# Kernel optimization log

Measured on AMD Instinct MI355X. Metric: run time of the kernel, lower is better.

Reference implementation:

```python
import jax, jax.numpy as jnp
import numpy as np

BINS = 10


def _neg_pearson(p, t):
    # global standardization (torch.std default is unbiased, ddof=1)
    p = (p - p.mean()) / p.std(ddof=1)
    t = (t - t.mean()) / t.std(ddof=1)
    N = p.shape[1]
    sx = p.sum(1); sy = t.sum(1)
    sxy = (p * t).sum(1)
    sx2 = (p * p).sum(1); sy2 = (t * t).sum(1)
    pear = (N * sxy - sx * sy) / jnp.sqrt((N * sx2 - sx**2) * (N * sy2 - sy**2))
    return (1.0 - pear).mean()


def _hann(N):
    # torch.hann_window is periodic: 0.5*(1 - cos(2*pi*n/N))
    return 0.5 * (1.0 - jnp.cos(2.0 * jnp.pi * jnp.arange(N, dtype=jnp.float32) / N))


def _phase_correlation(x, t):
    # torch.stft with n_fft=seq_len, center=False, hann window -> single frame = rfft(x*hann)
    N = x.shape[1]
    w = _hann(N)
    xf = jnp.fft.rfft(x * w, axis=1)   # [B, N//2+1]
    tf = jnp.fft.rfft(t * w, axis=1)
    corr = xf * jnp.conj(tf)
    corr = corr / jnp.abs(corr)        # phase-only correlation
    cm = jnp.fft.irfft(corr, n=N, axis=1)  # [B, N]
    idx = jnp.argmax(cm, axis=1)
    return 1.0 - jnp.mean(jnp.cos(2.0 * jnp.pi * idx / N))


def _power_spectrum(x, t):
    xp = jnp.abs(jnp.fft.rfft(x, axis=1)) ** 2
    tp = jnp.abs(jnp.fft.rfft(t, axis=1)) ** 2
    return jnp.mean(jnp.abs(xp - tp)) / jnp.mean(tp)


def _mutual_information(x, y, bins=BINS):
    B, S = x.shape
    xmin = x.min(1); xmax = x.max(1)
    ymin = y.min(1); ymax = y.max(1)
    bwx = (xmax - xmin) / bins
    bwy = (ymax - ymin) / bins
    ix = jnp.clip(((x - xmin[:, None]) / bwx[:, None]).astype(jnp.int32), 0, bins - 1)
    iy = jnp.clip(((y - ymin[:, None]) / bwy[:, None]).astype(jnp.int32), 0, bins - 1)
    flat = ix * bins + iy  # [B, S]
    # vectorized 2D histogram via scatter-add (replaces the python double loop)
    hist = jax.vmap(lambda f: jnp.zeros(bins * bins, jnp.float32).at[f].add(1.0))(flat)
    hist = hist.reshape(B, bins, bins)
    hx = hist.sum(2); hy = hist.sum(1)
    denom = B * S  # NOTE: original normalizes by batch*seq (faithful reproduction)
    px = hx / denom; py = hy / denom; pxy = hist / denom
    eps = 1e-8
    mi = (pxy * jnp.log((pxy + eps) / (px[:, :, None] * py[:, None, :] + eps))).sum((1, 2))
    hxe = -(px * jnp.log(px + eps)).sum(1)
    hye = -(py * jnp.log(py + eps)).sum(1)
    nmi = mi / ((hxe + hye) / 2.0)
    return 1.0 - nmi.mean()


def setup_inputs() -> dict:
    key = jax.random.key(0)
    k1, k2 = jax.random.split(key)
    return {
        "predictions": jax.random.normal(k1, (2, 512, 16384), dtype=jnp.float32),
        "targets": jax.random.normal(k2, (512, 16384), dtype=jnp.float32),
        "i": 0,
        "epoch": 700,
    }


def reference(predictions, targets, i, epoch):
    p = predictions[i]  # [B, S]
    loss = _neg_pearson(p, targets)
    if epoch >= 400:
        loss = loss + _phase_correlation(p, targets)
        loss = loss + _power_spectrum(p, targets)
    if epoch >= 700:
        loss = loss + _mutual_information(p, targets)
    return loss
```

## Files before the change

kernel.cpp:

```cpp
#include <hip/hip_runtime.h>
#include <math.h>

#define BB 512
#define SS 16384
#define TPIF 6.28318530717958647692f

#define PD(i) ((i) + ((i) >> 4) + ((i) >> 8))
#define NPD 17472
#define BBASE 8200

__device__ __forceinline__ int sp(int k) {
    int s = ((k & 7) << 11) + (((k >> 3) & 7) << 8) + (((k >> 6) & 7) << 5)
          + (((k >> 9) & 7) << 2) + ((k >> 12) & 3);
    return PD(s);
}


template <int SGN, int LOG2Q, bool DOMI = false>
__device__ __forceinline__ void stage_dif8(float2* sz, int t,
                                           float x0 = 0.f, float sbx = 0.f,
                                           float y0 = 0.f, float sby = 0.f,
                                           int* hsub = nullptr) {
    constexpr int Q = 1 << LOG2Q;
    constexpr int DQ = Q + (Q >> 4) + (Q >> 8);
    const float sg = (float)SGN;
    const float r2 = 0.70710678118654752f;
    float arev = sg * (float)(t & (Q - 1)) * (1.0f / (8.0f * (float)Q));
    float cb = __builtin_amdgcn_cosf(arev);
    float sb = __builtin_amdgcn_sinf(arev);
    #pragma unroll 1
    for (int c = 0; c < 2; ++c) {
        const int j = t + (c << 10);
        const int g = j >> LOG2Q;
        const int p = j & (Q - 1);
        const int i0 = PD((g << (LOG2Q + 3)) + p);
        int idx[8];
        #pragma unroll
        for (int k = 0; k < 8; ++k)
            idx[k] = (LOG2Q >= 4) ? (i0 + k * DQ) : (i0 + 4 * k + (k >> 2));
        float2 z[8];
        #pragma unroll
        for (int k = 0; k < 8; ++k) z[k] = sz[idx[k]];
        if constexpr (DOMI) {
            #pragma unroll
            for (int k = 0; k < 8; ++k) {
                int ix = (int)((z[k].x - x0) * sbx); ix = min(max(ix, 0), 9);
                int iy = (int)((z[k].y - y0) * sby); iy = min(max(iy, 0), 9);
                atomicAdd(&hsub[ix * 10 + iy], 1);
            }
        }
        float2 a0, a1, a2, a3, b0, b1, b2, b3;
        a0 = make_float2(z[0].x + z[4].x, z[0].y + z[4].y);
        b0 = make_float2(z[0].x - z[4].x, z[0].y - z[4].y);
        a1 = make_float2(z[1].x + z[5].x, z[1].y + z[5].y);
        b1 = make_float2(z[1].x - z[5].x, z[1].y - z[5].y);
        a2 = make_float2(z[2].x + z[6].x, z[2].y + z[6].y);
        b2 = make_float2(z[2].x - z[6].x, z[2].y - z[6].y);
        a3 = make_float2(z[3].x + z[7].x, z[3].y + z[7].y);
        b3 = make_float2(z[3].x - z[7].x, z[3].y - z[7].y);
        { float x = b1.x, y = b1.y; b1 = make_float2(r2 * (x - sg * y), r2 * (y + sg * x)); }
        { float x = b2.x, y = b2.y; b2 = make_float2(-sg * y, sg * x); }
        { float x = b3.x, y = b3.y; b3 = make_float2(-r2 * (x + sg * y), r2 * (sg * x - y)); }
        float2 o[8];
        {
            float t0r = a0.x + a2.x, t0i = a0.y + a2.y;
            float t1r = a0.x - a2.x, t1i = a0.y - a2.y;
            float t2r = a1.x + a3.x, t2i = a1.y + a3.y;
            float t3r = a1.x - a3.x, t3i = a1.y - a3.y;
            o[0] = make_float2(t0r + t2r, t0i + t2i);
            o[4] = make_float2(t0r - t2r, t0i - t2i);
            o[2] = make_float2(t1r - sg * t3i, t1i + sg * t3r);
            o[6] = make_float2(t1r + sg * t3i, t1i - sg * t3r);
        }
        {
            float t0r = b0.x + b2.x, t0i = b0.y + b2.y;
            float t1r = b0.x - b2.x, t1i = b0.y - b2.y;
            float t2r = b1.x + b3.x, t2i = b1.y + b3.y;
            float t3r = b1.x - b3.x, t3i = b1.y - b3.y;
            o[1] = make_float2(t0r + t2r, t0i + t2i);
            o[5] = make_float2(t0r - t2r, t0i - t2i);
            o[3] = make_float2(t1r - sg * t3i, t1i + sg * t3r);
            o[7] = make_float2(t1r + sg * t3i, t1i - sg * t3r);
        }
        sz[idx[0]] = o[0];
        float wr = cb, wi = sb;
        #pragma unroll
        for (int r = 1; r < 8; ++r) {
            sz[idx[r]] = make_float2(o[r].x * wr - o[r].y * wi,
                                     o[r].x * wi + o[r].y * wr);
            float nr = wr * cb - wi * sb, ni = wr * sb + wi * cb;
            wr = nr; wi = ni;
        }
        if constexpr (LOG2Q == 11) {
            const float cs = 0.92387953251128674f;
            const float sn = 0.38268343236508977f * (float)SGN;
            float nb = cb * cs - sb * sn, nsb = cb * sn + sb * cs;
            cb = nb; sb = nsb;
        }
    }
    __syncthreads();
}

template <int SGN>
__device__ __forceinline__ void stage_nt4(float2* sz, int t) {
    const float sg = (float)SGN;
    #pragma unroll 1
    for (int c = 0; c < 4; ++c) {
        const int j = t + (c << 10);
        const int i0 = 4 * j + (j >> 2) + (j >> 6);
        float2 z0 = sz[i0], z1 = sz[i0 + 1], z2 = sz[i0 + 2], z3 = sz[i0 + 3];
        float t0r = z0.x + z2.x, t0i = z0.y + z2.y;
        float t1r = z0.x - z2.x, t1i = z0.y - z2.y;
        float t2r = z1.x + z3.x, t2i = z1.y + z3.y;
        float t3r = z1.x - z3.x, t3i = z1.y - z3.y;
        sz[i0]     = make_float2(t0r + t2r, t0i + t2i);
        sz[i0 + 2] = make_float2(t0r - t2r, t0i - t2i);
        sz[i0 + 1] = make_float2(t1r - sg * t3i, t1i + sg * t3r);
        sz[i0 + 3] = make_float2(t1r + sg * t3i, t1i - sg * t3r);
    }
    __syncthreads();
}

template <int SGN, int LOG2Q>
__device__ __forceinline__ void stage8k_dif8(float2* bz, int t) {
    constexpr int Q = 1 << LOG2Q;
    constexpr int DQ = Q + (Q >> 4) + (Q >> 8);
    constexpr int CORR = (LOG2Q == 7) ? 1 : 0;
    const float sg = (float)SGN;
    const float r2 = 0.70710678118654752f;
    const int g = t >> LOG2Q;
    const int p = t & (Q - 1);
    const int i0 = PD((g << (LOG2Q + 3)) + p);
    int idx[8];
    #pragma unroll
    for (int k = 0; k < 8; ++k) idx[k] = i0 + k * DQ + CORR * (k >> 1);
    float2 z[8];
    #pragma unroll
    for (int k = 0; k < 8; ++k) z[k] = bz[idx[k]];
    float2 a0, a1, a2, a3, b0, b1, b2, b3;
    a0 = make_float2(z[0].x + z[4].x, z[0].y + z[4].y);
    b0 = make_float2(z[0].x - z[4].x, z[0].y - z[4].y);
    a1 = make_float2(z[1].x + z[5].x, z[1].y + z[5].y);
    b1 = make_float2(z[1].x - z[5].x, z[1].y - z[5].y);
    a2 = make_float2(z[2].x + z[6].x, z[2].y + z[6].y);
    b2 = make_float2(z[2].x - z[6].x, z[2].y - z[6].y);
    a3 = make_float2(z[3].x + z[7].x, z[3].y + z[7].y);
    b3 = make_float2(z[3].x - z[7].x, z[3].y - z[7].y);
    { float x = b1.x, y = b1.y; b1 = make_float2(r2 * (x - sg * y), r2 * (y + sg * x)); }
    { float x = b2.x, y = b2.y; b2 = make_float2(-sg * y, sg * x); }
    { float x = b3.x, y = b3.y; b3 = make_float2(-r2 * (x + sg * y), r2 * (sg * x - y)); }
    float2 o[8];
    {
        float t0r = a0.x + a2.x, t0i = a0.y + a2.y;
        float t1r = a0.x - a2.x, t1i = a0.y - a2.y;
        float t2r = a1.x + a3.x, t2i = a1.y + a3.y;
        float t3r = a1.x - a3.x, t3i = a1.y - a3.y;
        o[0] = make_float2(t0r + t2r, t0i + t2i);
        o[4] = make_float2(t0r - t2r, t0i - t2i);
        o[2] = make_float2(t1r - sg * t3i, t1i + sg * t3r);
        o[6] = make_float2(t1r + sg * t3i, t1i - sg * t3r);
    }
    {
        float t0r = b0.x + b2.x, t0i = b0.y + b2.y;
        float t1r = b0.x - b2.x, t1i = b0.y - b2.y;
        float t2r = b1.x + b3.x, t2i = b1.y + b3.y;
        float t3r = b1.x - b3.x, t3i = b1.y - b3.y;
        o[1] = make_float2(t0r + t2r, t0i + t2i);
        o[5] = make_float2(t0r - t2r, t0i - t2i);
        o[3] = make_float2(t1r - sg * t3i, t1i + sg * t3r);
        o[7] = make_float2(t1r + sg * t3i, t1i - sg * t3r);
    }
    const float arev = sg * (float)p * (1.0f / (8.0f * (float)Q));
    const float cb = __builtin_amdgcn_cosf(arev);
    const float sb = __builtin_amdgcn_sinf(arev);
    bz[idx[0]] = o[0];
    float wr = cb, wi = sb;
    #pragma unroll
    for (int r = 1; r < 8; ++r) {
        bz[idx[r]] = make_float2(o[r].x * wr - o[r].y * wi,
                                 o[r].x * wi + o[r].y * wr);
        float nr = wr * cb - wi * sb, ni = wr * sb + wi * cb;
        wr = nr; wi = ni;
    }
    __syncthreads();
}

__device__ __forceinline__ void inv_first(float2* sz, float2* bz, int t) {
    const float r2 = 0.70710678118654752f;
    float2 z[8];
    {
        float a0w = (float)t * (1.0f / 16384.0f);
        float wr = __builtin_amdgcn_cosf(a0w);
        float wi = __builtin_amdgcn_sinf(a0w);
        const float cs = 0.92387953251128674f;
        const float sn = 0.38268343236508977f;
        #pragma unroll
        for (int c = 0; c < 8; ++c) {
            int m = t + (c << 10);
            float2 cm = sz[m];
            float2 cn = sz[8192 - m];
            float Ax = cm.x + cn.x, Ay = cm.y - cn.y;
            float Dx = cm.x - cn.x, Dy = cm.y + cn.y;
            float WDx = Dx * wr - Dy * wi;
            float WDy = Dx * wi + Dy * wr;
            z[c] = make_float2(Ax - WDy, Ay + WDx);
            float nr = wr * cs - wi * sn, ni = wr * sn + wi * cs;
            wr = nr; wi = ni;
        }
    }
    const float sg = 1.0f;
    const int i0 = PD(t);
    float2 a0, a1, a2, a3, b0, b1, b2, b3;
    a0 = make_float2(z[0].x + z[4].x, z[0].y + z[4].y);
    b0 = make_float2(z[0].x - z[4].x, z[0].y - z[4].y);
    a1 = make_float2(z[1].x + z[5].x, z[1].y + z[5].y);
    b1 = make_float2(z[1].x - z[5].x, z[1].y - z[5].y);
    a2 = make_float2(z[2].x + z[6].x, z[2].y + z[6].y);
    b2 = make_float2(z[2].x - z[6].x, z[2].y - z[6].y);
    a3 = make_float2(z[3].x + z[7].x, z[3].y + z[7].y);
    b3 = make_float2(z[3].x - z[7].x, z[3].y - z[7].y);
    { float x = b1.x, y = b1.y; b1 = make_float2(r2 * (x - sg * y), r2 * (y + sg * x)); }
    { float x = b2.x, y = b2.y; b2 = make_float2(-sg * y, sg * x); }
    { float x = b3.x, y = b3.y; b3 = make_float2(-r2 * (x + sg * y), r2 * (sg * x - y)); }
    float2 o[8];
    {
        float t0r = a0.x + a2.x, t0i = a0.y + a2.y;
        float t1r = a0.x - a2.x, t1i = a0.y - a2.y;
        float t2r = a1.x + a3.x, t2i = a1.y + a3.y;
        float t3r = a1.x - a3.x, t3i = a1.y - a3.y;
        o[0] = make_float2(t0r + t2r, t0i + t2i);
        o[4] = make_float2(t0r - t2r, t0i - t2i);
        o[2] = make_float2(t1r - sg * t3i, t1i + sg * t3r);
        o[6] = make_float2(t1r + sg * t3i, t1i - sg * t3r);
    }
    {
        float t0r = b0.x + b2.x, t0i = b0.y + b2.y;
        float t1r = b0.x - b2.x, t1i = b0.y - b2.y;
        float t2r = b1.x + b3.x, t2i = b1.y + b3.y;
        float t3r = b1.x - b3.x, t3i = b1.y - b3.y;
        o[1] = make_float2(t0r + t2r, t0i + t2i);
        o[5] = make_float2(t0r - t2r, t0i - t2i);
        o[3] = make_float2(t1r - sg * t3i, t1i + sg * t3r);
        o[7] = make_float2(t1r + sg * t3i, t1i - sg * t3r);
    }
    const float arev = (float)t * (1.0f / 8192.0f);
    const float cb = __builtin_amdgcn_cosf(arev);
    const float sb = __builtin_amdgcn_sinf(arev);
    bz[i0] = o[0];
    float wr = cb, wi = sb;
    #pragma unroll
    for (int r = 1; r < 8; ++r) {
        bz[i0 + r * 1092] = make_float2(o[r].x * wr - o[r].y * wi,
                                        o[r].x * wi + o[r].y * wr);
        float nr = wr * cb - wi * sb, ni = wr * sb + wi * cb;
        wr = nr; wi = ni;
    }
    __syncthreads();
}

template <int SGN>
__device__ __forceinline__ void stage8k_dif4(float2* bz, int t) {
    const float sg = (float)SGN;
    const float a = sg * (float)(t & 3) * (1.0f / 16.0f);
    const float cb = __builtin_amdgcn_cosf(a);
    const float sb = __builtin_amdgcn_sinf(a);
    const float w2r = cb * cb - sb * sb, w2i = 2.0f * cb * sb;
    const float w3r = cb * w2r - sb * w2i, w3i = cb * w2i + sb * w2r;
    #pragma unroll 1
    for (int c = 0; c < 2; ++c) {
        const int j = t + (c << 10);
        const int g = j >> 2;
        const int p = j & 3;
        const int i0 = PD((g << 4) + p);
        float2 z0 = bz[i0], z1 = bz[i0 + 4], z2 = bz[i0 + 8], z3 = bz[i0 + 12];
        float t0r = z0.x + z2.x, t0i = z0.y + z2.y;
        float t1r = z0.x - z2.x, t1i = z0.y - z2.y;
        float t2r = z1.x + z3.x, t2i = z1.y + z3.y;
        float t3r = z1.x - z3.x, t3i = z1.y - z3.y;
        float b0r = t0r + t2r, b0i = t0i + t2i;
        float b2r = t0r - t2r, b2i = t0i - t2i;
        float b1r = t1r - sg * t3i, b1i = t1i + sg * t3r;
        float b3r = t1r + sg * t3i, b3i = t1i - sg * t3r;
        bz[i0]      = make_float2(b0r, b0i);
        bz[i0 + 4]  = make_float2(b1r * cb - b1i * sb,   b1r * sb + b1i * cb);
        bz[i0 + 8]  = make_float2(b2r * w2r - b2i * w2i, b2r * w2i + b2i * w2r);
        bz[i0 + 12] = make_float2(b3r * w3r - b3i * w3i, b3r * w3i + b3i * w3r);
    }
    __syncthreads();
}

__device__ __forceinline__ void inv_last_argmax(float2* bz, int t, float* pbv, int* pbi) {
    float bv = -3.4e38f; int bi = 0;
    #pragma unroll 1
    for (int c = 0; c < 2; ++c) {
        const int j = t + (c << 10);
        const int i0 = 4 * j + (j >> 2) + (j >> 6);
        float2 z0 = bz[i0], z1 = bz[i0 + 1], z2 = bz[i0 + 2], z3 = bz[i0 + 3];
        float t0r = z0.x + z2.x, t0i = z0.y + z2.y;
        float t1r = z0.x - z2.x, t1i = z0.y - z2.y;
        float t2r = z1.x + z3.x, t2i = z1.y + z3.y;
        float t3r = z1.x - z3.x, t3i = z1.y - z3.y;
        float re[4], im[4];
        re[0] = t0r + t2r; im[0] = t0i + t2i;
        re[1] = t1r - t3i; im[1] = t1i + t3r;
        re[2] = t0r - t2r; im[2] = t0i - t2i;
        re[3] = t1r + t3i; im[3] = t1i - t3r;
        const int nb = (j >> 8) + ((j >> 5) & 7) * 8 + ((j >> 2) & 7) * 64 + (j & 3) * 512;
        #pragma unroll
        for (int k = 0; k < 4; ++k) {
            int n2 = (nb + 2048 * k) << 1;
            if (re[k] > bv || (re[k] == bv && n2 < bi)) { bv = re[k]; bi = n2; }
            if (im[k] > bv || (im[k] == bv && n2 + 1 < bi)) { bv = im[k]; bi = n2 + 1; }
        }
    }
    *pbv = bv; *pbi = bi;
}

__global__ __launch_bounds__(1024, 4) void k_main(const float* __restrict__ pred,
                                                  const float* __restrict__ targ,
                                                  const int* __restrict__ ip,
                                                  float* __restrict__ wpear,
                                                  float* __restrict__ wcos,
                                                  double* __restrict__ wnum,
                                                  double* __restrict__ wden,
                                                  float* __restrict__ wnmi) {
    __shared__ float2 sz[NPD];
    __shared__ double dpart[16 * 5];
    __shared__ float fpart[16 * 4];
    __shared__ int   subhist[1600];
    __shared__ float hxm[10], hym[10];
    __shared__ float mterm[128];
    __shared__ float sbounds[4];
    __shared__ float svalw[16];
    __shared__ int   sidxw[16];

    const int row = blockIdx.x;
    const int t = threadIdx.x;
    const int w = t >> 6;
    const int lane = t & 63;
    float2* bz = &sz[BBASE];

    const float* xg = pred + (size_t)ip[0] * (size_t)BB * SS + (size_t)row * SS;
    const float* yg = targ + (size_t)row * SS;

    {
        const float4* xg4 = reinterpret_cast<const float4*>(xg);
        const float4* yg4 = reinterpret_cast<const float4*>(yg);
        float sx = 0, sy = 0, sxy = 0, sxx = 0, syy = 0;
        float xmn = 3.4e38f, xmx = -3.4e38f, ymn = 3.4e38f, ymx = -3.4e38f;
        #pragma unroll
        for (int m2 = 0; m2 < 4; ++m2) {
            int idx = t + (m2 << 10);
            float4 a = xg4[idx];
            float4 b = yg4[idx];
            int n0 = idx << 2;
            sz[PD(n0 + 0)] = make_float2(a.x, b.x);
            sz[PD(n0 + 1)] = make_float2(a.y, b.y);
            sz[PD(n0 + 2)] = make_float2(a.z, b.z);
            sz[PD(n0 + 3)] = make_float2(a.w, b.w);
            float av[4] = {a.x, a.y, a.z, a.w};
            float bv[4] = {b.x, b.y, b.z, b.w};
            #pragma unroll
            for (int c = 0; c < 4; ++c) {
                float aa = av[c], bb = bv[c];
                sx += aa; sy += bb;
                sxy += aa * bb;
                sxx += aa * aa;
                syy += bb * bb;
                xmn = fminf(xmn, aa); xmx = fmaxf(xmx, aa);
                ymn = fminf(ymn, bb); ymx = fmaxf(ymx, bb);
            }
        }
        #pragma unroll
        for (int o = 32; o > 0; o >>= 1) {
            sx += __shfl_down(sx, o, 64);  sy += __shfl_down(sy, o, 64);
            sxy += __shfl_down(sxy, o, 64);
            sxx += __shfl_down(sxx, o, 64); syy += __shfl_down(syy, o, 64);
            xmn = fminf(xmn, __shfl_down(xmn, o, 64));
            xmx = fmaxf(xmx, __shfl_down(xmx, o, 64));
            ymn = fminf(ymn, __shfl_down(ymn, o, 64));
            ymx = fmaxf(ymx, __shfl_down(ymx, o, 64));
        }
        if (lane == 0) {
            dpart[w*5+0] = (double)sx; dpart[w*5+1] = (double)sy;
            dpart[w*5+2] = (double)sxy;
            dpart[w*5+3] = (double)sxx; dpart[w*5+4] = (double)syy;
            fpart[w*4+0] = xmn; fpart[w*4+1] = xmx; fpart[w*4+2] = ymn; fpart[w*4+3] = ymx;
        }
    }
    subhist[t] = 0;
    if (t < 576) subhist[1024 + t] = 0;
    __syncthreads();
    if (t == 0) {
        double v0=0,v1=0,v2=0,v3=0,v4=0;
        float b0=fpart[0], b1=fpart[1], b2=fpart[2], b3=fpart[3];
        for (int q = 0; q < 16; ++q) {
            v0 += dpart[q*5]; v1 += dpart[q*5+1]; v2 += dpart[q*5+2];
            v3 += dpart[q*5+3]; v4 += dpart[q*5+4];
            b0 = fminf(b0, fpart[q*4]);   b1 = fmaxf(b1, fpart[q*4+1]);
            b2 = fminf(b2, fpart[q*4+2]); b3 = fmaxf(b3, fpart[q*4+3]);
        }
        double N = (double)SS;
        double num = N * v2 - v0 * v1;
        double den = sqrt((N * v3 - v0 * v0) * (N * v4 - v1 * v1));
        wpear[row] = (float)(1.0 - num / den);
        sbounds[0] = b0; sbounds[1] = 10.0f / (b1 - b0);
        sbounds[2] = b2; sbounds[3] = 10.0f / (b3 - b2);
    }
    __syncthreads();

    {
        const float x0 = sbounds[0], sbx = sbounds[1];
        const float y0 = sbounds[2], sby = sbounds[3];
        int* hsub = subhist + w * 100;
        stage_dif8<-1, 11, true>(sz, t, x0, sbx, y0, sby, hsub);
    }

    if (t < 100) {
        int s = 0;
        #pragma unroll
        for (int q = 0; q < 16; ++q) s += subhist[t + 100 * q];
        subhist[t] = s;
    }
    __syncthreads();
    if (t < 10) {
        int s1 = 0, s2 = 0;
        for (int j = 0; j < 10; ++j) { s1 += subhist[t*10+j]; s2 += subhist[j*10+t]; }
        hxm[t] = (float)s1; hym[t] = (float)s2;
    }
    __syncthreads();
    {
        float term = 0.0f;
        if (t < 100) {
            const float denom = 8388608.0f, eps = 1e-8f;
            float pxy = (float)subhist[t] / denom;
            float px = hxm[t / 10] / denom, py = hym[t % 10] / denom;
            term = pxy * logf((pxy + eps) / (px * py + eps));
        }
        if (t < 128) mterm[t] = (t < 100) ? term : 0.0f;
    }
    __syncthreads();
    if (t == 0) {
        const float denom = 8388608.0f, eps = 1e-8f;
        float mi = 0.0f;
        for (int q = 0; q < 100; ++q) mi += mterm[q];
        float hxe = 0.0f, hye = 0.0f;
        for (int q = 0; q < 10; ++q) {
            float px = hxm[q] / denom, py = hym[q] / denom;
            hxe -= px * logf(px + eps);
            hye -= py * logf(py + eps);
        }
        wnmi[row] = mi / (0.5f * (hxe + hye));
    }

    stage_dif8<-1,  8>(sz, t);
    stage_dif8<-1,  5>(sz, t);
    stage_dif8<-1,  2>(sz, t);
    stage_nt4<-1>(sz, t);

    {
        double anum = 0.0, aden = 0.0;
        float crv[8], civ[8];
        #pragma unroll 1
        for (int m = 0; m < 8; ++m) {
            int k = t + (m << 10);
            int km = (SS - k) & (SS - 1);
            float2 za = sz[sp(k)];
            float2 zb = sz[sp(km)];
            float ar  = za.x, ai  = za.y;
            float cr0 = zb.x, ci0 = zb.y;
            float xr = 0.5f * (ar + cr0), xi = 0.5f * (ai - ci0);
            float yr = 0.5f * (ai + ci0), yi = 0.5f * (cr0 - ar);
            float xp = xr * xr + xi * xi;
            float tp = yr * yr + yi * yi;
            anum += (double)fabsf(xp - tp);
            aden += (double)tp;
            float2 zap, zam, zbp, zbm;
            zap.x = __shfl_down(za.x, 1, 64); zap.y = __shfl_down(za.y, 1, 64);
            zam.x = __shfl_up(za.x, 1, 64);   zam.y = __shfl_up(za.y, 1, 64);
            zbm.x = __shfl_down(zb.x, 1, 64); zbm.y = __shfl_down(zb.y, 1, 64);
            zbp.x = __shfl_up(zb.x, 1, 64);   zbp.y = __shfl_up(zb.y, 1, 64);
            if (lane == 63) {
                zap = sz[sp((k + 1) & (SS - 1))];
                zbm = sz[sp((km - 1) & (SS - 1))];
            }
            if (lane == 0) {
                zam = sz[sp((k - 1) & (SS - 1))];
                zbp = sz[sp((km + 1) & (SS - 1))];
            }
            float zwr = 0.5f * ar  - 0.25f * (zap.x + zam.x);
            float zwi = 0.5f * ai  - 0.25f * (zap.y + zam.y);
            float vwr = 0.5f * cr0 - 0.25f * (zbp.x + zbm.x);
            float vwi = 0.5f * ci0 - 0.25f * (zbp.y + zbm.y);
            float xwr = 0.5f * (zwr + vwr), xwi = 0.5f * (zwi - vwi);
            float ywr = 0.5f * (zwi + vwi), ywi = 0.5f * (vwr - zwr);
            float cr = xwr * ywr + xwi * ywi;
            float ci = xwi * ywr - xwr * ywi;
            float mag = sqrtf(cr * cr + ci * ci);
            crv[m] = cr / mag; civ[m] = ci / mag;
        }
        float c8 = 0.0f;
        if (t == 0) {
            float2 z0 = sz[sp(8192)];
            float2 zp = sz[sp(8193)];
            float2 zm = sz[sp(8191)];
            float ar = z0.x, ai = z0.y;
            anum += (double)fabsf(ar * ar - ai * ai);
            aden += (double)(ai * ai);
            float zwr = 0.5f * ar - 0.25f * (zp.x + zm.x);
            float zwi = 0.5f * ai - 0.25f * (zp.y + zm.y);
            float pr = zwr * zwi;
            c8 = pr / fabsf(pr);
        }
        #pragma unroll
        for (int o = 32; o > 0; o >>= 1) {
            anum += __shfl_down(anum, o, 64);
            aden += __shfl_down(aden, o, 64);
        }
        if (lane == 0) { dpart[w*2] = anum; dpart[w*2+1] = aden; }
        __syncthreads();
        #pragma unroll
        for (int m = 0; m < 8; ++m) {
            int k = t + (m << 10);
            sz[k] = make_float2(crv[m], civ[m]);
        }
        if (t == 0) {
            sz[8192] = make_float2(c8, 0.0f);
            double a = 0, b = 0;
            for (int q2_ = 0; q2_ < 16; ++q2_) { a += dpart[q2_*2]; b += dpart[q2_*2+1]; }
            wnum[row] = a; wden[row] = b;
        }
    }
    __syncthreads();

    inv_first(sz, bz, t);
    stage8k_dif8<1,  7>(bz, t);
    stage8k_dif8<1,  4>(bz, t);
    stage8k_dif4<1>(bz, t);
    {
        float bv; int bi;
        inv_last_argmax(bz, t, &bv, &bi);
        #pragma unroll
        for (int o = 32; o > 0; o >>= 1) {
            float v2 = __shfl_down(bv, o, 64);
            int i2 = __shfl_down(bi, o, 64);
            if (v2 > bv || (v2 == bv && i2 < bi)) { bv = v2; bi = i2; }
        }
        if (lane == 0) { svalw[w] = bv; sidxw[w] = bi; }
    }
    __syncthreads();
    if (t == 0) {
        float bv = svalw[0]; int bi = sidxw[0];
        for (int q = 1; q < 16; ++q) {
            if (svalw[q] > bv || (svalw[q] == bv && sidxw[q] < bi)) { bv = svalw[q]; bi = sidxw[q]; }
        }
        wcos[row] = cosf(TPIF * (float)bi / 16384.0f);
    }
}

__global__ __launch_bounds__(512) void k_combine(const float* __restrict__ wpear,
                                                 const float* __restrict__ wcos,
                                                 const double* __restrict__ wnum,
                                                 const double* __restrict__ wden,
                                                 const float* __restrict__ wnmi,
                                                 const int* __restrict__ ep,
                                                 float* __restrict__ out) {
    __shared__ double dp[8 * 5];
    const int tid = threadIdx.x;
    const int w = tid >> 6, lane = tid & 63;
    double v0 = (double)wpear[tid], v1 = (double)wcos[tid];
    double v2 = wnum[tid], v3 = wden[tid], v4 = (double)wnmi[tid];
    #pragma unroll
    for (int o = 32; o > 0; o >>= 1) {
        v0 += __shfl_down(v0, o, 64); v1 += __shfl_down(v1, o, 64);
        v2 += __shfl_down(v2, o, 64); v3 += __shfl_down(v3, o, 64);
        v4 += __shfl_down(v4, o, 64);
    }
    if (lane == 0) {
        dp[w*5+0] = v0; dp[w*5+1] = v1; dp[w*5+2] = v2; dp[w*5+3] = v3; dp[w*5+4] = v4;
    }
    __syncthreads();
    if (tid == 0) {
        double s0=0,s1=0,s2=0,s3=0,s4=0;
        for (int q = 0; q < 8; ++q) {
            s0 += dp[q*5]; s1 += dp[q*5+1]; s2 += dp[q*5+2]; s3 += dp[q*5+3]; s4 += dp[q*5+4];
        }
        int epoch = ep[0];
        double loss = s0 / 512.0;
        if (epoch >= 400) {
            loss += 1.0 - s1 / 512.0;
            loss += s2 / s3;
        }
        if (epoch >= 700) {
            loss += 1.0 - s4 / 512.0;
        }
        out[0] = (float)loss;
    }
}

extern "C" void kernel_launch(void* const* d_in, const int* in_sizes, int n_in,
                              void* d_out, int out_size, void* d_ws, size_t ws_size,
                              hipStream_t stream) {
    const float* pred = (const float*)d_in[0];
    const float* targ = (const float*)d_in[1];
    const int* ip = (const int*)d_in[2];
    const int* ep = (const int*)d_in[3];
    float* out = (float*)d_out;

    double* wnum = (double*)d_ws;
    double* wden = wnum + BB;
    float* wpear = (float*)(wden + BB);
    float* wcos = wpear + BB;
    float* wnmi = wcos + BB;

    k_main<<<dim3(BB), dim3(1024), 0, stream>>>(pred, targ, ip, wpear, wcos, wnum, wden, wnmi);
    k_combine<<<dim3(1), dim3(512), 0, stream>>>(wpear, wcos, wnum, wden, wnmi, ep, out);
}
```

Measured before the change: 181.8 us.

## Interleave MI histogram reductions with FFT stages to drop extra barriers

The standalone barriers between the mutual-information histogram reduction steps are removed. Those steps are now interleaved with the subsequent radix-8 FFT stages, so each stage's barrier also covers a histogram step. Each FFT stage now issues both chunks' LDS loads before computing and shares one twiddle computation between them. Several small loops are fully unrolled. This raises register pressure and relies on the FFT stages not touching the histogram buffers.

```diff
diff --git a/kernel.cpp b/kernel.cpp
--- a/kernel.cpp
+++ b/kernel.cpp
@@ -16,127 +16,13 @@
 }
 
 
-template <int SGN, int LOG2Q, bool DOMI = false>
-__device__ __forceinline__ void stage_dif8(float2* sz, int t,
-                                           float x0 = 0.f, float sbx = 0.f,
-                                           float y0 = 0.f, float sby = 0.f,
-                                           int* hsub = nullptr) {
+template <int SGN, int LOG2Q>
+__device__ __forceinline__ void bfly8_store(float2* sz, const float2* z, int i0,
+                                            float cb, float sb) {
     constexpr int Q = 1 << LOG2Q;
     constexpr int DQ = Q + (Q >> 4) + (Q >> 8);
     const float sg = (float)SGN;
     const float r2 = 0.70710678118654752f;
-    float arev = sg * (float)(t & (Q - 1)) * (1.0f / (8.0f * (float)Q));
-    float cb = __builtin_amdgcn_cosf(arev);
-    float sb = __builtin_amdgcn_sinf(arev);
-    #pragma unroll 1
-    for (int c = 0; c < 2; ++c) {
-        const int j = t + (c << 10);
-        const int g = j >> LOG2Q;
-        const int p = j & (Q - 1);
-        const int i0 = PD((g << (LOG2Q + 3)) + p);
-        int idx[8];
-        #pragma unroll
-        for (int k = 0; k < 8; ++k)
-            idx[k] = (LOG2Q >= 4) ? (i0 + k * DQ) : (i0 + 4 * k + (k >> 2));
-        float2 z[8];
-        #pragma unroll
-        for (int k = 0; k < 8; ++k) z[k] = sz[idx[k]];
-        if constexpr (DOMI) {
-            #pragma unroll
-            for (int k = 0; k < 8; ++k) {
-                int ix = (int)((z[k].x - x0) * sbx); ix = min(max(ix, 0), 9);
-                int iy = (int)((z[k].y - y0) * sby); iy = min(max(iy, 0), 9);
-                atomicAdd(&hsub[ix * 10 + iy], 1);
-            }
-        }
-        float2 a0, a1, a2, a3, b0, b1, b2, b3;
-        a0 = make_float2(z[0].x + z[4].x, z[0].y + z[4].y);
-        b0 = make_float2(z[0].x - z[4].x, z[0].y - z[4].y);
-        a1 = make_float2(z[1].x + z[5].x, z[1].y + z[5].y);
-        b1 = make_float2(z[1].x - z[5].x, z[1].y - z[5].y);
-        a2 = make_float2(z[2].x + z[6].x, z[2].y + z[6].y);
-        b2 = make_float2(z[2].x - z[6].x, z[2].y - z[6].y);
-        a3 = make_float2(z[3].x + z[7].x, z[3].y + z[7].y);
-        b3 = make_float2(z[3].x - z[7].x, z[3].y - z[7].y);
-        { float x = b1.x, y = b1.y; b1 = make_float2(r2 * (x - sg * y), r2 * (y + sg * x)); }
-        { float x = b2.x, y = b2.y; b2 = make_float2(-sg * y, sg * x); }
-        { float x = b3.x, y = b3.y; b3 = make_float2(-r2 * (x + sg * y), r2 * (sg * x - y)); }
-        float2 o[8];
-        {
-            float t0r = a0.x + a2.x, t0i = a0.y + a2.y;
-            float t1r = a0.x - a2.x, t1i = a0.y - a2.y;
-            float t2r = a1.x + a3.x, t2i = a1.y + a3.y;
-            float t3r = a1.x - a3.x, t3i = a1.y - a3.y;
-            o[0] = make_float2(t0r + t2r, t0i + t2i);
-            o[4] = make_float2(t0r - t2r, t0i - t2i);
-            o[2] = make_float2(t1r - sg * t3i, t1i + sg * t3r);
-            o[6] = make_float2(t1r + sg * t3i, t1i - sg * t3r);
-        }
-        {
-            float t0r = b0.x + b2.x, t0i = b0.y + b2.y;
-            float t1r = b0.x - b2.x, t1i = b0.y - b2.y;
-            float t2r = b1.x + b3.x, t2i = b1.y + b3.y;
-            float t3r = b1.x - b3.x, t3i = b1.y - b3.y;
-            o[1] = make_float2(t0r + t2r, t0i + t2i);
-            o[5] = make_float2(t0r - t2r, t0i - t2i);
-            o[3] = make_float2(t1r - sg * t3i, t1i + sg * t3r);
-            o[7] = make_float2(t1r + sg * t3i, t1i - sg * t3r);
-        }
-        sz[idx[0]] = o[0];
-        float wr = cb, wi = sb;
-        #pragma unroll
-        for (int r = 1; r < 8; ++r) {
-            sz[idx[r]] = make_float2(o[r].x * wr - o[r].y * wi,
-                                     o[r].x * wi + o[r].y * wr);
-            float nr = wr * cb - wi * sb, ni = wr * sb + wi * cb;
-            wr = nr; wi = ni;
-        }
-        if constexpr (LOG2Q == 11) {
-            const float cs = 0.92387953251128674f;
-            const float sn = 0.38268343236508977f * (float)SGN;
-            float nb = cb * cs - sb * sn, nsb = cb * sn + sb * cs;
-            cb = nb; sb = nsb;
-        }
-    }
-    __syncthreads();
-}
-
-template <int SGN>
-__device__ __forceinline__ void stage_nt4(float2* sz, int t) {
-    const float sg = (float)SGN;
-    #pragma unroll 1
-    for (int c = 0; c < 4; ++c) {
-        const int j = t + (c << 10);
-        const int i0 = 4 * j + (j >> 2) + (j >> 6);
-        float2 z0 = sz[i0], z1 = sz[i0 + 1], z2 = sz[i0 + 2], z3 = sz[i0 + 3];
-        float t0r = z0.x + z2.x, t0i = z0.y + z2.y;
-        float t1r = z0.x - z2.x, t1i = z0.y - z2.y;
-        float t2r = z1.x + z3.x, t2i = z1.y + z3.y;
-        float t3r = z1.x - z3.x, t3i = z1.y - z3.y;
-        sz[i0]     = make_float2(t0r + t2r, t0i + t2i);
-        sz[i0 + 2] = make_float2(t0r - t2r, t0i - t2i);
-        sz[i0 + 1] = make_float2(t1r - sg * t3i, t1i + sg * t3r);
-        sz[i0 + 3] = make_float2(t1r + sg * t3i, t1i - sg * t3r);
-    }
-    __syncthreads();
-}
-
-template <int SGN, int LOG2Q>
-__device__ __forceinline__ void stage8k_dif8(float2* bz, int t) {
-    constexpr int Q = 1 << LOG2Q;
-    constexpr int DQ = Q + (Q >> 4) + (Q >> 8);
-    constexpr int CORR = (LOG2Q == 7) ? 1 : 0;
-    const float sg = (float)SGN;
-    const float r2 = 0.70710678118654752f;
-    const int g = t >> LOG2Q;
-    const int p = t & (Q - 1);
-    const int i0 = PD((g << (LOG2Q + 3)) + p);
-    int idx[8];
-    #pragma unroll
-    for (int k = 0; k < 8; ++k) idx[k] = i0 + k * DQ + CORR * (k >> 1);
-    float2 z[8];
-    #pragma unroll
-    for (int k = 0; k < 8; ++k) z[k] = bz[idx[k]];
     float2 a0, a1, a2, a3, b0, b1, b2, b3;
     a0 = make_float2(z[0].x + z[4].x, z[0].y + z[4].y);
     b0 = make_float2(z[0].x - z[4].x, z[0].y - z[4].y);
@@ -170,46 +56,115 @@
         o[3] = make_float2(t1r - sg * t3i, t1i + sg * t3r);
         o[7] = make_float2(t1r + sg * t3i, t1i - sg * t3r);
     }
+    sz[(LOG2Q >= 4) ? i0 : i0] = o[0];
+    float wr = cb, wi = sb;
+    #pragma unroll
+    for (int r = 1; r < 8; ++r) {
+        const int ir = (LOG2Q >= 4) ? (i0 + r * DQ) : (i0 + 4 * r + (r >> 2));
+        sz[ir] = make_float2(o[r].x * wr - o[r].y * wi,
+                             o[r].x * wi + o[r].y * wr);
+        float nr = wr * cb - wi * sb, ni = wr * sb + wi * cb;
+        wr = nr; wi = ni;
+    }
+}
+
+template <int SGN, int LOG2Q>
+__device__ __forceinline__ void stage_dif8(float2* sz, int t) {
+    constexpr int Q = 1 << LOG2Q;
+    constexpr int DQ = Q + (Q >> 4) + (Q >> 8);
+    const int gA = t >> LOG2Q;
+    const int p  = t & (Q - 1);
+    const int i0A = PD((gA << (LOG2Q + 3)) + p);
+    const int gB = (t + 1024) >> LOG2Q;
+    const int i0B = PD((gB << (LOG2Q + 3)) + p);
+    float2 zA[8], zB[8];
+    #pragma unroll
+    for (int k = 0; k < 8; ++k)
+        zA[k] = sz[(LOG2Q >= 4) ? (i0A + k * DQ) : (i0A + 4 * k + (k >> 2))];
+    #pragma unroll
+    for (int k = 0; k < 8; ++k)
+        zB[k] = sz[(LOG2Q >= 4) ? (i0B + k * DQ) : (i0B + 4 * k + (k >> 2))];
+    const float arev = (float)SGN * (float)p * (1.0f / (8.0f * (float)Q));
+    const float cb = __builtin_amdgcn_cosf(arev);
+    const float sb = __builtin_amdgcn_sinf(arev);
+    bfly8_store<SGN, LOG2Q>(sz, zA, i0A, cb, sb);
+    bfly8_store<SGN, LOG2Q>(sz, zB, i0B, cb, sb);
+    __syncthreads();
+}
+
+__device__ __forceinline__ void stage1_mi(float2* sz, int t, float x0, float sbx,
+                                          float y0, float sby, int* hsub) {
+    constexpr int LOG2Q = 11;
+    constexpr int Q = 1 << LOG2Q;
+    constexpr int DQ = Q + (Q >> 4) + (Q >> 8);
+    const float sg = -1.0f;
+    const float r2 = 0.70710678118654752f;
+    float arev = sg * (float)(t & (Q - 1)) * (1.0f / (8.0f * (float)Q));
+    float cb = __builtin_amdgcn_cosf(arev);
+    float sb = __builtin_amdgcn_sinf(arev);
+    #pragma unroll 1
+    for (int c = 0; c < 2; ++c) {
+        const int j = t + (c << 10);
+        const int g = j >> LOG2Q;
+        const int p = j & (Q - 1);
+        const int i0 = PD((g << (LOG2Q + 3)) + p);
+        float2 z[8];
+        #pragma unroll
+        for (int k = 0; k < 8; ++k) z[k] = sz[i0 + k * DQ];
+        #pragma unroll
+        for (int k = 0; k < 8; ++k) {
+            int ix = (int)((z[k].x - x0) * sbx); ix = min(max(ix, 0), 9);
+            int iy = (int)((z[k].y - y0) * sby); iy = min(max(iy, 0), 9);
+            atomicAdd(&hsub[ix * 10 + iy], 1);
+        }
+        bfly8_store<-1, LOG2Q>(sz, z, i0, cb, sb);
+        const float cs = 0.92387953251128674f;
+        const float sn = -0.38268343236508977f;
+        float nb = cb * cs - sb * sn, nsb = cb * sn + sb * cs;
+        cb = nb; sb = nsb;
+    }
+    __syncthreads();
+}
+
+template <int SGN>
+__device__ __forceinline__ void stage_nt4(float2* sz, int t) {
+    const float sg = (float)SGN;
+    #pragma unroll
+    for (int c = 0; c < 4; ++c) {
+        const int j = t + (c << 10);
+        const int i0 = 4 * j + (j >> 2) + (j >> 6);
+        float2 z0 = sz[i0], z1 = sz[i0 + 1], z2 = sz[i0 + 2], z3 = sz[i0 + 3];
+        float t0r = z0.x + z2.x, t0i = z0.y + z2.y;
+        float t1r = z0.x - z2.x, t1i = z0.y - z2.y;
+        float t2r = z1.x + z3.x, t2i = z1.y + z3.y;
+        float t3r = z1.x - z3.x, t3i = z1.y - z3.y;
+        sz[i0]     = make_float2(t0r + t2r, t0i + t2i);
+        sz[i0 + 2] = make_float2(t0r - t2r, t0i - t2i);
+        sz[i0 + 1] = make_float2(t1r - sg * t3i, t1i + sg * t3r);
+        sz[i0 + 3] = make_float2(t1r + sg * t3i, t1i - sg * t3r);
+    }
+    __syncthreads();
+}
+
+template <int SGN, int LOG2Q>
+__device__ __forceinline__ void stage8k_dif8(float2* bz, int t) {
+    constexpr int Q = 1 << LOG2Q;
+    constexpr int DQ = Q + (Q >> 4) + (Q >> 8);
+    constexpr int CORR = (LOG2Q == 7) ? 1 : 0;
+    const float sg = (float)SGN;
+    const int g = t >> LOG2Q;
+    const int p = t & (Q - 1);
+    const int i0 = PD((g << (LOG2Q + 3)) + p);
+    int idx[8];
+    #pragma unroll
+    for (int k = 0; k < 8; ++k) idx[k] = i0 + k * DQ + CORR * (k >> 1);
+    float2 z[8];
+    #pragma unroll
+    for (int k = 0; k < 8; ++k) z[k] = bz[idx[k]];
     const float arev = sg * (float)p * (1.0f / (8.0f * (float)Q));
     const float cb = __builtin_amdgcn_cosf(arev);
     const float sb = __builtin_amdgcn_sinf(arev);
-    bz[idx[0]] = o[0];
-    float wr = cb, wi = sb;
-    #pragma unroll
-    for (int r = 1; r < 8; ++r) {
-        bz[idx[r]] = make_float2(o[r].x * wr - o[r].y * wi,
-                                 o[r].x * wi + o[r].y * wr);
-        float nr = wr * cb - wi * sb, ni = wr * sb + wi * cb;
-        wr = nr; wi = ni;
-    }
-    __syncthreads();
-}
-
-__device__ __forceinline__ void inv_first(float2* sz, float2* bz, int t) {
     const float r2 = 0.70710678118654752f;
-    float2 z[8];
-    {
-        float a0w = (float)t * (1.0f / 16384.0f);
-        float wr = __builtin_amdgcn_cosf(a0w);
-        float wi = __builtin_amdgcn_sinf(a0w);
-        const float cs = 0.92387953251128674f;
-        const float sn = 0.38268343236508977f;
-        #pragma unroll
-        for (int c = 0; c < 8; ++c) {
-            int m = t + (c << 10);
-            float2 cm = sz[m];
-            float2 cn = sz[8192 - m];
-            float Ax = cm.x + cn.x, Ay = cm.y - cn.y;
-            float Dx = cm.x - cn.x, Dy = cm.y + cn.y;
-            float WDx = Dx * wr - Dy * wi;
-            float WDy = Dx * wi + Dy * wr;
-            z[c] = make_float2(Ax - WDy, Ay + WDx);
-            float nr = wr * cs - wi * sn, ni = wr * sn + wi * cs;
-            wr = nr; wi = ni;
-        }
-    }
-    const float sg = 1.0f;
-    const int i0 = PD(t);
     float2 a0, a1, a2, a3, b0, b1, b2, b3;
     a0 = make_float2(z[0].x + z[4].x, z[0].y + z[4].y);
     b0 = make_float2(z[0].x - z[4].x, z[0].y - z[4].y);
@@ -243,18 +198,44 @@
         o[3] = make_float2(t1r - sg * t3i, t1i + sg * t3r);
         o[7] = make_float2(t1r + sg * t3i, t1i - sg * t3r);
     }
+    bz[idx[0]] = o[0];
+    float wr = cb, wi = sb;
+    #pragma unroll
+    for (int r = 1; r < 8; ++r) {
+        bz[idx[r]] = make_float2(o[r].x * wr - o[r].y * wi,
+                                 o[r].x * wi + o[r].y * wr);
+        float nr = wr * cb - wi * sb, ni = wr * sb + wi * cb;
+        wr = nr; wi = ni;
+    }
+    __syncthreads();
+}
+
+__device__ __forceinline__ void inv_first(float2* sz, float2* bz, int t) {
+    float2 z[8];
+    {
+        float a0w = (float)t * (1.0f / 16384.0f);
+        float wr = __builtin_amdgcn_cosf(a0w);
+        float wi = __builtin_amdgcn_sinf(a0w);
+        const float cs = 0.92387953251128674f;
+        const float sn = 0.38268343236508977f;
+        #pragma unroll
+        for (int c = 0; c < 8; ++c) {
+            int m = t + (c << 10);
+            float2 cm = sz[m];
+            float2 cn = sz[8192 - m];
+            float Ax = cm.x + cn.x, Ay = cm.y - cn.y;
+            float Dx = cm.x - cn.x, Dy = cm.y + cn.y;
+            float WDx = Dx * wr - Dy * wi;
+            float WDy = Dx * wi + Dy * wr;
+            z[c] = make_float2(Ax - WDy, Ay + WDx);
+            float nr = wr * cs - wi * sn, ni = wr * sn + wi * cs;
+            wr = nr; wi = ni;
+        }
+    }
     const float arev = (float)t * (1.0f / 8192.0f);
     const float cb = __builtin_amdgcn_cosf(arev);
     const float sb = __builtin_amdgcn_sinf(arev);
-    bz[i0] = o[0];
-    float wr = cb, wi = sb;
-    #pragma unroll
-    for (int r = 1; r < 8; ++r) {
-        bz[i0 + r * 1092] = make_float2(o[r].x * wr - o[r].y * wi,
-                                        o[r].x * wi + o[r].y * wr);
-        float nr = wr * cb - wi * sb, ni = wr * sb + wi * cb;
-        wr = nr; wi = ni;
-    }
+    bfly8_store<1, 10>(bz, z, PD(t), cb, sb);
     __syncthreads();
 }
 
@@ -266,7 +247,7 @@
     const float sb = __builtin_amdgcn_sinf(a);
     const float w2r = cb * cb - sb * sb, w2i = 2.0f * cb * sb;
     const float w3r = cb * w2r - sb * w2i, w3i = cb * w2i + sb * w2r;
-    #pragma unroll 1
+    #pragma unroll
     for (int c = 0; c < 2; ++c) {
         const int j = t + (c << 10);
         const int g = j >> 2;
@@ -291,7 +272,7 @@
 
 __device__ __forceinline__ void inv_last_argmax(float2* bz, int t, float* pbv, int* pbi) {
     float bv = -3.4e38f; int bi = 0;
-    #pragma unroll 1
+    #pragma unroll
     for (int c = 0; c < 2; ++c) {
         const int j = t + (c << 10);
         const int i0 = 4 * j + (j >> 2) + (j >> 6);
@@ -409,12 +390,8 @@
     }
     __syncthreads();
 
-    {
-        const float x0 = sbounds[0], sbx = sbounds[1];
-        const float y0 = sbounds[2], sby = sbounds[3];
-        int* hsub = subhist + w * 100;
-        stage_dif8<-1, 11, true>(sz, t, x0, sbx, y0, sby, hsub);
-    }
+    stage1_mi(sz, t, sbounds[0], sbounds[1], sbounds[2], sbounds[3],
+              subhist + w * 100);
 
     if (t < 100) {
         int s = 0;
@@ -422,13 +399,13 @@
         for (int q = 0; q < 16; ++q) s += subhist[t + 100 * q];
         subhist[t] = s;
     }
-    __syncthreads();
+    stage_dif8<-1, 8>(sz, t);
     if (t < 10) {
         int s1 = 0, s2 = 0;
         for (int j = 0; j < 10; ++j) { s1 += subhist[t*10+j]; s2 += subhist[j*10+t]; }
         hxm[t] = (float)s1; hym[t] = (float)s2;
     }
-    __syncthreads();
+    stage_dif8<-1, 5>(sz, t);
     {
         float term = 0.0f;
         if (t < 100) {
@@ -439,7 +416,7 @@
         }
         if (t < 128) mterm[t] = (t < 100) ? term : 0.0f;
     }
-    __syncthreads();
+    stage_dif8<-1, 2>(sz, t);
     if (t == 0) {
         const float denom = 8388608.0f, eps = 1e-8f;
         float mi = 0.0f;
@@ -452,10 +429,6 @@
         }
         wnmi[row] = mi / (0.5f * (hxe + hye));
     }
-
-    stage_dif8<-1,  8>(sz, t);
-    stage_dif8<-1,  5>(sz, t);
-    stage_dif8<-1,  2>(sz, t);
     stage_nt4<-1>(sz, t);
 
     {
```

After: 176.1 us. 3.1% less time.
